# Performance work log

Measured on AMD Instinct MI355X. Metric: run time of the kernel, lower is better.

## Reference

```python
import jax, jax.numpy as jnp
import numpy as np

EPS = 1e-5      # BatchNorm1d eps
THETA = 1.0     # spike threshold
ALPHA = 5.0     # ATan surrogate alpha

@jax.custom_vjp
def atan_spike(x):
    # forward: heaviside; backward: ATan surrogate gradient
    return (x > 0).astype(x.dtype)

def _spike_fwd(x):
    return atan_spike(x), x

def _spike_bwd(x, g):
    return (g * ALPHA / (2.0 * (1.0 + (jnp.pi / 2.0 * ALPHA * x) ** 2)),)

atan_spike.defvjp(_spike_fwd, _spike_bwd)

def _lif_layer(x, W, beta_raw, gamma, bias, readout):
    # x: [T,B,J], W: [I,J]
    x = jnp.einsum('tbj,ij->tbi', x, W)
    # BatchNorm1d over (T*B) samples, per channel (training-mode batch stats)
    mean = jnp.mean(x, axis=(0, 1))
    var = jnp.var(x, axis=(0, 1))
    x = (x - mean) * jax.lax.rsqrt(var + EPS) * gamma + bias
    beta = jax.nn.sigmoid(beta_raw)
    B, I = x.shape[1], x.shape[2]
    U0 = jnp.zeros((B, I), x.dtype)
    if readout:
        def step(Ut, xt):
            Ut = beta * Ut + (1.0 - beta) * xt
            return Ut, Ut
        _, o = jax.lax.scan(step, U0, x)
    else:
        def step(carry, xt):
            Ut, St = carry
            Ut = beta * (Ut - THETA * St) + (1.0 - beta) * xt
            St = atan_spike(Ut - THETA)
            return (Ut, St), St
        _, o = jax.lax.scan(step, (U0, U0), x)
    return o  # [T,B,I]

def setup_inputs():
    key = jax.random.key(0)
    ks = jax.random.split(key, 8)
    B, T, J, H, O = 128, 512, 700, 512, 20
    def kaiming(k, out_dim, in_dim):
        # kaiming_uniform_(a=sqrt(5)) -> bound = 1/sqrt(fan_in)
        bound = 1.0 / np.sqrt(in_dim)
        return jax.random.uniform(k, (out_dim, in_dim), jnp.float32, -bound, bound)
    return {
        'x': jax.random.normal(ks[0], (B, T, J), jnp.float32),
        'W1': kaiming(ks[1], H, J),
        'beta1': jax.random.uniform(ks[2], (H,), jnp.float32, 0.0, 1.0),
        'g1': jnp.ones((H,), jnp.float32),
        'b1': jnp.zeros((H,), jnp.float32),
        'W2': kaiming(ks[3], H, H),
        'beta2': jax.random.uniform(ks[4], (H,), jnp.float32, 0.0, 1.0),
        'g2': jnp.ones((H,), jnp.float32),
        'b2': jnp.zeros((H,), jnp.float32),
        'Wr': kaiming(ks[5], O, H),
        'betar': jax.random.uniform(ks[6], (O,), jnp.float32, 0.0, 1.0),
        'gr': jnp.ones((O,), jnp.float32),
        'br': jnp.zeros((O,), jnp.float32),
    }

def reference(x, W1, beta1, g1, b1, W2, beta2, g2, b2, Wr, betar, gr, br):
    h = jnp.transpose(x, (1, 0, 2))  # [B,T,J] -> [T,B,J]
    h = _lif_layer(h, W1, beta1, g1, b1, readout=False)
    h = _lif_layer(h, W2, beta2, g2, b2, readout=False)
    h = _lif_layer(h, Wr, betar, gr, br, readout=True)
    p = jax.nn.softmax(h, axis=2)  # [T,B,O]
    return p.sum(axis=0)           # [B,O]
```

## Files before the change

### kernel.cpp

```cpp
#include <hip/hip_runtime.h>
#include <math.h>

typedef _Float16 f16_t;
typedef _Float16 f16x8 __attribute__((ext_vector_type(8)));
typedef float f32x4 __attribute__((ext_vector_type(4)));

constexpr int Bn = 128;
constexpr int Tn = 512;
constexpr int Jn = 700;
constexpr int Jp = 704;
constexpr int Hn = 512;
constexpr int On = 20;
constexpr int Mn = Bn * Tn;

#define LDS_U32(p) ((__attribute__((address_space(3))) uint32_t*)(p))
#define GLB_U32(p) ((const __attribute__((address_space(1))) uint32_t*)(p))

template <int NT, int MODE>
__global__ __launch_bounds__(512, 4) void gemm_snn(
    const f16_t* __restrict__ A, const f16_t* __restrict__ W,
    float* __restrict__ C, float* __restrict__ s_out, float* __restrict__ q_out,
    int LDA, int LDW, int KP, int pairs, int Nout, float outScale)
{
    constexpr int JT = 2 * NT;
    constexpr int ASL = (MODE == 0) ? 2 : 1;
    __shared__ __align__(16) f16_t sA[ASL * 4096];
    __shared__ __align__(16) f16_t sW[2 * NT * 4096];

    const int tid  = threadIdx.x;
    const int bm   = blockIdx.y * 128;
    const int bn   = blockIdx.x * (NT * 128);
    const int lane = tid & 63;
    const int wv   = tid >> 6;
    const int wm   = (wv & 1) * 64;
    const int wn   = (wv >> 1) * (NT * 32);
    const int fr   = lane & 15;
    const int quad = lane >> 4;
    const int srow = lane >> 2;
    const int scol = (((lane & 3) ^ ((lane >> 3) & 3)) * 8);
    const int ksw  = ((quad ^ ((fr >> 1) & 3)) * 8);

    f32x4 acc[4][JT];
#pragma unroll
    for (int i = 0; i < 4; ++i)
#pragma unroll
        for (int j = 0; j < JT; ++j) acc[i][j] = {0.f, 0.f, 0.f, 0.f};

    for (int p = 0; p < pairs; ++p) {
#pragma unroll
        for (int cc = 0; cc < ASL; ++cc) {
            const int c  = wv + cc * 8;
            const int s  = c >> 3;
            const int cr = (c & 7) * 16;
            const int kA = (MODE == 0) ? p * 64 + s * 32 : p * 32;
            const uint32_t off = __builtin_amdgcn_readfirstlane(s * 8192 + cr * 64);
            const f16_t* gp = A + (size_t)(bm + cr + srow) * LDA + kA + scol;
            __builtin_amdgcn_global_load_lds(GLB_U32(gp), LDS_U32((char*)sA + off), 16, 0, 0);
        }
#pragma unroll
        for (int cc = 0; cc < 2 * NT; ++cc) {
            const int c   = wv + cc * 8;
            const int h   = c / (NT * 8);
            const int rem = c % (NT * 8);
            const int nt  = rem >> 3;
            const int cr  = (rem & 7) * 16;
            const int kW  = (MODE == 0) ? p * 64 + h * 32 : h * KP + p * 32;
            const uint32_t off = __builtin_amdgcn_readfirstlane((h * NT + nt) * 8192 + cr * 64);
            const f16_t* gp = W + (size_t)(bn + nt * 128 + cr + srow) * LDW + kW + scol;
            __builtin_amdgcn_global_load_lds(GLB_U32(gp), LDS_U32((char*)sW + off), 16, 0, 0);
        }
        __syncthreads();

        f16x8 av[4];
#pragma unroll
        for (int h = 0; h < 2; ++h) {
            if (h == 0 || MODE == 0) {
                const int s = (MODE == 0) ? h : 0;
#pragma unroll
                for (int i = 0; i < 4; ++i)
                    av[i] = *(const f16x8*)&sA[s * 4096 + (wm + i * 16 + fr) * 32 + ksw];
            }
            f16x8 wf[JT];
#pragma unroll
            for (int jt = 0; jt < JT; ++jt) {
                const int n = wn + jt * 16 + fr;
                wf[jt] = *(const f16x8*)&sW[(h * NT + (n >> 7)) * 4096 + (n & 127) * 32 + ksw];
            }
#pragma unroll
            for (int i = 0; i < 4; ++i)
#pragma unroll
                for (int jt = 0; jt < JT; ++jt)
                    acc[i][jt] = __builtin_amdgcn_mfma_f32_16x16x32_f16(av[i], wf[jt], acc[i][jt], 0, 0, 0);
        }
        __syncthreads();
    }

#pragma unroll
    for (int jt = 0; jt < JT; ++jt) {
        const int gcol = bn + wn + jt * 16 + fr;
        float s = 0.f, q = 0.f;
        if (gcol < Nout) {
#pragma unroll
            for (int i = 0; i < 4; ++i) {
#pragma unroll
                for (int rg = 0; rg < 4; ++rg) {
                    const float v = acc[i][jt][rg] * outScale;
                    C[(size_t)(bm + wm + i * 16 + quad * 4 + rg) * Nout + gcol] = v;
                    s += v;
                    q += v * v;
                }
            }
        }
        s += __shfl_xor(s, 16); s += __shfl_xor(s, 32);
        q += __shfl_xor(q, 16); q += __shfl_xor(q, 32);
        if (quad == 0 && gcol < Nout) {
            atomicAdd(&s_out[gcol], s);
            atomicAdd(&q_out[gcol], q);
        }
    }
}

__global__ __launch_bounds__(256) void conv_a1(const float* __restrict__ x,
                                               f16_t* __restrict__ A1) {
    const int idx = blockIdx.x * 256 + threadIdx.x;
    const int m = idx / 88, g = idx % 88;
    const int k8 = g * 8;
    const float* rp = x + (size_t)m * Jn + k8;
    float f[8];
    if (k8 + 8 <= Jn) {
        const float4 v0 = *(const float4*)rp;
        const float4 v1 = *(const float4*)(rp + 4);
        f[0] = v0.x; f[1] = v0.y; f[2] = v0.z; f[3] = v0.w;
        f[4] = v1.x; f[5] = v1.y; f[6] = v1.z; f[7] = v1.w;
    } else {
#pragma unroll
        for (int e = 0; e < 8; ++e) f[e] = (k8 + e < Jn) ? rp[e] : 0.f;
    }
    f16x8 hv;
#pragma unroll
    for (int e = 0; e < 8; ++e) hv[e] = (f16_t)(f[e] * 32.f);
    *(f16x8*)&A1[(size_t)m * Jp + k8] = hv;
}

__global__ __launch_bounds__(256) void conv_w1(const float* __restrict__ Wsrc,
                                               f16_t* __restrict__ Wo) {
    const int idx = blockIdx.x * 256 + threadIdx.x;
    if (idx >= Hn * 88) return;
    const int n = idx / 88, g = idx % 88;
    const int k8 = g * 8;
    const float* rp = Wsrc + (size_t)n * Jn + k8;
    f16x8 hv;
#pragma unroll
    for (int e = 0; e < 8; ++e) {
        const float f = (k8 + e < Jn) ? rp[e] : 0.f;
        hv[e] = (f16_t)(f * 64.f);
    }
    *(f16x8*)&Wo[(size_t)n * Jp + k8] = hv;
}

__global__ __launch_bounds__(256) void split_w(const float* __restrict__ Wsrc,
                                               f16_t* __restrict__ Wo,
                                               int N, int K, int KP, int NP) {
    const int idx = blockIdx.x * 256 + threadIdx.x;
    if (idx >= NP * KP) return;
    const int n = idx / KP, k = idx % KP;
    const float f = (n < N && k < K) ? Wsrc[(size_t)n * K + k] * 64.f : 0.f;
    const f16_t hi = (f16_t)f;
    const f16_t lo = (f16_t)(f - (float)hi);
    Wo[(size_t)n * (2 * KP) + k] = hi;
    Wo[(size_t)n * (2 * KP) + KP + k] = lo;
}

__global__ __launch_bounds__(256) void lif_scan1(const float* __restrict__ X,
                                                 f16_t* __restrict__ S_out,
                                                 const float* __restrict__ sums,
                                                 const float* __restrict__ sumsq,
                                                 const float* __restrict__ beta_raw,
                                                 const float* __restrict__ gamma,
                                                 const float* __restrict__ bias) {
    const int gid = blockIdx.x * 256 + threadIdx.x;
    const int b = gid >> 9;
    const int i = gid & 511;

    const float invM = 1.f / (float)Mn;
    const float mean = sums[i] * invM;
    const float var  = sumsq[i] * invM - mean * mean;
    const float inv  = rsqrtf(var + 1e-5f);
    const float g    = gamma[i] * inv;
    const float bi   = bias[i] - mean * g;
    const float bt   = 1.f / (1.f + expf(-beta_raw[i]));
    const float ob   = 1.f - bt;

    const float* xp = X + (size_t)b * Tn * Hn + i;
    f16_t* sp = S_out + (size_t)b * Tn * Hn + i;

    float U = 0.f, Sp = 0.f;
#pragma unroll 8
    for (int t = 0; t < Tn; ++t) {
        const float xt = xp[(size_t)t * Hn] * g + bi;
        U = bt * (U - Sp) + ob * xt;
        Sp = (U > 1.0f) ? 1.0f : 0.0f;
        sp[(size_t)t * Hn] = (f16_t)Sp;
    }
}

__global__ __launch_bounds__(256) void readout_kernel(const float* __restrict__ A,
                                                      const float* __restrict__ sums,
                                                      const float* __restrict__ sumsq,
                                                      const float* __restrict__ beta_raw,
                                                      const float* __restrict__ gamma,
                                                      const float* __restrict__ bias,
                                                      float* __restrict__ out) {
    __shared__ float xs[Tn * On];
    __shared__ float gsh[On], bsh[On], betash[On];
    __shared__ float red[4][On];

    const int b = blockIdx.x;
    const int tid = threadIdx.x;

    if (tid < On) {
        const float invM = 1.f / (float)Mn;
        const float mean = sums[tid] * invM;
        const float var = sumsq[tid] * invM - mean * mean;
        const float inv = rsqrtf(var + 1e-5f);
        const float g = gamma[tid] * inv;
        gsh[tid] = g;
        bsh[tid] = bias[tid] - mean * g;
        betash[tid] = 1.f / (1.f + expf(-beta_raw[tid]));
    }
    __syncthreads();

    const float* Ab = A + (size_t)b * Tn * On;
    for (int idx = tid; idx < Tn * On; idx += 256) {
        const int o = idx % On;
        xs[idx] = Ab[idx] * gsh[o] + bsh[o];
    }
    __syncthreads();

    if (tid < On) {
        const float beta = betash[tid], omb = 1.f - beta;
        float U = 0.f;
        for (int t = 0; t < Tn; ++t) {
            U = beta * U + omb * xs[t * On + tid];
            xs[t * On + tid] = U;
        }
    }
    __syncthreads();

    float part[On];
#pragma unroll
    for (int o = 0; o < On; ++o) part[o] = 0.f;

    for (int t = tid; t < Tn; t += 256) {
        float v[On];
        float m = -1e30f;
#pragma unroll
        for (int o = 0; o < On; ++o) {
            v[o] = xs[t * On + o];
            m = fmaxf(m, v[o]);
        }
        float s = 0.f;
#pragma unroll
        for (int o = 0; o < On; ++o) {
            v[o] = expf(v[o] - m);
            s += v[o];
        }
        const float rs = 1.f / s;
#pragma unroll
        for (int o = 0; o < On; ++o) part[o] += v[o] * rs;
    }

#pragma unroll
    for (int o = 0; o < On; ++o) {
#pragma unroll
        for (int off = 32; off > 0; off >>= 1) part[o] += __shfl_down(part[o], off);
    }
    const int lane = tid & 63, wid = tid >> 6;
    if (lane == 0) {
#pragma unroll
        for (int o = 0; o < On; ++o) red[wid][o] = part[o];
    }
    __syncthreads();
    if (tid < On) out[b * On + tid] = red[0][tid] + red[1][tid] + red[2][tid] + red[3][tid];
}

extern "C" void kernel_launch(void* const* d_in, const int* in_sizes, int n_in,
                              void* d_out, int out_size, void* d_ws, size_t ws_size,
                              hipStream_t stream) {
    const float* x   = (const float*)d_in[0];
    const float* W1  = (const float*)d_in[1];
    const float* be1 = (const float*)d_in[2];
    const float* g1  = (const float*)d_in[3];
    const float* b1  = (const float*)d_in[4];
    const float* W2  = (const float*)d_in[5];
    const float* be2 = (const float*)d_in[6];
    const float* b2g = (const float*)d_in[7];
    const float* b2  = (const float*)d_in[8];
    const float* Wr  = (const float*)d_in[9];
    const float* ber = (const float*)d_in[10];
    const float* gr  = (const float*)d_in[11];
    const float* br  = (const float*)d_in[12];
    float* out = (float*)d_out;

    char* ws = (char*)d_ws;
    const size_t r0Bytes   = (size_t)Mn * Jp * sizeof(f16_t);
    const size_t bufCBytes = (size_t)Mn * Hn * sizeof(float);
    f16_t* A1   = (f16_t*)ws;
    f16_t* bufS = (f16_t*)ws;
    float* bufC = (float*)(ws + r0Bytes);
    char*  p    = ws + r0Bytes + bufCBytes;
    float* bufR = (float*)p;              p += (size_t)Mn * On * sizeof(float);
    f16_t* W1h  = (f16_t*)p;              p += (size_t)Hn * Jp * sizeof(f16_t);
    f16_t* W2s  = (f16_t*)p;              p += (size_t)Hn * (2 * Hn) * sizeof(f16_t);
    f16_t* Wrs  = (f16_t*)p;              p += (size_t)128 * (2 * Hn) * sizeof(f16_t);
    float* stats = (float*)p;
    float* s1 = stats;       float* q1 = s1 + Hn;
    float* s2 = q1 + Hn;     float* q2 = s2 + Hn;
    float* s3 = q2 + Hn;     float* q3 = s3 + 32;

    hipMemsetAsync(stats, 0, (4 * Hn + 64) * sizeof(float), stream);

    conv_a1<<<(Mn * 88) / 256, 256, 0, stream>>>(x, A1);
    conv_w1<<<(Hn * 88 + 255) / 256, 256, 0, stream>>>(W1, W1h);
    split_w<<<(Hn * Hn + 255) / 256, 256, 0, stream>>>(W2, W2s, Hn, Hn, Hn, Hn);
    split_w<<<(128 * Hn + 255) / 256, 256, 0, stream>>>(Wr, Wrs, On, Hn, Hn, 128);

    gemm_snn<2, 0><<<dim3(2, Mn / 128), 512, 0, stream>>>(A1, W1h, bufC, s1, q1,
        Jp, Jp, 0, Jp / 64, Hn, 1.f / 2048.f);
    lif_scan1<<<Mn * Hn / (512 * 256), 256, 0, stream>>>(bufC, bufS, s1, q1, be1, g1, b1);

    gemm_snn<2, 1><<<dim3(2, Mn / 128), 512, 0, stream>>>(bufS, W2s, bufC, s2, q2,
        Hn, 2 * Hn, Hn, Hn / 32, Hn, 1.f / 64.f);
    lif_scan1<<<Mn * Hn / (512 * 256), 256, 0, stream>>>(bufC, bufS, s2, q2, be2, b2g, b2);

    gemm_snn<1, 1><<<dim3(1, Mn / 128), 512, 0, stream>>>(bufS, Wrs, bufR, s3, q3,
        Hn, 2 * Hn, Hn, Hn / 32, On, 1.f / 64.f);
    readout_kernel<<<Bn, 256, 0, stream>>>(bufR, s3, q3, ber, gr, br, out);
}
```

Measured before the change: 588.7 us.

## Drop hi/lo weight split, unscaled f16 GEMMs, swizzled grid, paired-channel LIF scan

```diff
diff --git a/kernel.cpp b/kernel.cpp
--- a/kernel.cpp
+++ b/kernel.cpp
@@ -2,6 +2,7 @@
 #include <math.h>
 
 typedef _Float16 f16_t;
+typedef _Float16 f16x2 __attribute__((ext_vector_type(2)));
 typedef _Float16 f16x8 __attribute__((ext_vector_type(8)));
 typedef float f32x4 __attribute__((ext_vector_type(4)));
 
@@ -16,20 +17,28 @@
 #define LDS_U32(p) ((__attribute__((address_space(3))) uint32_t*)(p))
 #define GLB_U32(p) ((const __attribute__((address_space(1))) uint32_t*)(p))
 
-template <int NT, int MODE>
-__global__ __launch_bounds__(512, 4) void gemm_snn(
+template <int NT, bool SWZ>
+__global__ __launch_bounds__(512, 4) void gemm_f16(
     const f16_t* __restrict__ A, const f16_t* __restrict__ W,
     float* __restrict__ C, float* __restrict__ s_out, float* __restrict__ q_out,
-    int LDA, int LDW, int KP, int pairs, int Nout, float outScale)
+    int LDA, int LDW, int pairs, int Nout)
 {
     constexpr int JT = 2 * NT;
-    constexpr int ASL = (MODE == 0) ? 2 : 1;
-    __shared__ __align__(16) f16_t sA[ASL * 4096];
+    __shared__ __align__(16) f16_t sA[2 * 4096];
     __shared__ __align__(16) f16_t sW[2 * NT * 4096];
 
+    int bx, by;
+    if (SWZ) {
+        const int g = blockIdx.x;
+        by = (g >> 4) * 8 + (g & 7);
+        bx = (g >> 3) & 1;
+    } else {
+        bx = blockIdx.x;
+        by = blockIdx.y;
+    }
     const int tid  = threadIdx.x;
-    const int bm   = blockIdx.y * 128;
-    const int bn   = blockIdx.x * (NT * 128);
+    const int bm   = by * 128;
+    const int bn   = bx * (NT * 128);
     const int lane = tid & 63;
     const int wv   = tid >> 6;
     const int wm   = (wv & 1) * 64;
@@ -48,11 +57,11 @@
 
     for (int p = 0; p < pairs; ++p) {
 #pragma unroll
-        for (int cc = 0; cc < ASL; ++cc) {
+        for (int cc = 0; cc < 2; ++cc) {
             const int c  = wv + cc * 8;
             const int s  = c >> 3;
             const int cr = (c & 7) * 16;
-            const int kA = (MODE == 0) ? p * 64 + s * 32 : p * 32;
+            const int kA = p * 64 + s * 32;
             const uint32_t off = __builtin_amdgcn_readfirstlane(s * 8192 + cr * 64);
             const f16_t* gp = A + (size_t)(bm + cr + srow) * LDA + kA + scol;
             __builtin_amdgcn_global_load_lds(GLB_U32(gp), LDS_U32((char*)sA + off), 16, 0, 0);
@@ -64,22 +73,19 @@
             const int rem = c % (NT * 8);
             const int nt  = rem >> 3;
             const int cr  = (rem & 7) * 16;
-            const int kW  = (MODE == 0) ? p * 64 + h * 32 : h * KP + p * 32;
+            const int kW  = p * 64 + h * 32;
             const uint32_t off = __builtin_amdgcn_readfirstlane((h * NT + nt) * 8192 + cr * 64);
             const f16_t* gp = W + (size_t)(bn + nt * 128 + cr + srow) * LDW + kW + scol;
             __builtin_amdgcn_global_load_lds(GLB_U32(gp), LDS_U32((char*)sW + off), 16, 0, 0);
         }
         __syncthreads();
 
-        f16x8 av[4];
 #pragma unroll
         for (int h = 0; h < 2; ++h) {
-            if (h == 0 || MODE == 0) {
-                const int s = (MODE == 0) ? h : 0;
-#pragma unroll
-                for (int i = 0; i < 4; ++i)
-                    av[i] = *(const f16x8*)&sA[s * 4096 + (wm + i * 16 + fr) * 32 + ksw];
-            }
+            f16x8 av[4];
+#pragma unroll
+            for (int i = 0; i < 4; ++i)
+                av[i] = *(const f16x8*)&sA[h * 4096 + (wm + i * 16 + fr) * 32 + ksw];
             f16x8 wf[JT];
 #pragma unroll
             for (int jt = 0; jt < JT; ++jt) {
@@ -104,7 +110,7 @@
             for (int i = 0; i < 4; ++i) {
 #pragma unroll
                 for (int rg = 0; rg < 4; ++rg) {
-                    const float v = acc[i][jt][rg] * outScale;
+                    const float v = acc[i][jt][rg];
                     C[(size_t)(bm + wm + i * 16 + quad * 4 + rg) * Nout + gcol] = v;
                     s += v;
                     q += v * v;
@@ -120,8 +126,8 @@
     }
 }
 
-__global__ __launch_bounds__(256) void conv_a1(const float* __restrict__ x,
-                                               f16_t* __restrict__ A1) {
+__global__ __launch_bounds__(256) void conv_x(const float* __restrict__ x,
+                                              f16_t* __restrict__ A1) {
     const int idx = blockIdx.x * 256 + threadIdx.x;
     const int m = idx / 88, g = idx % 88;
     const int k8 = g * 8;
@@ -138,69 +144,69 @@
     }
     f16x8 hv;
 #pragma unroll
-    for (int e = 0; e < 8; ++e) hv[e] = (f16_t)(f[e] * 32.f);
+    for (int e = 0; e < 8; ++e) hv[e] = (f16_t)f[e];
     *(f16x8*)&A1[(size_t)m * Jp + k8] = hv;
 }
 
-__global__ __launch_bounds__(256) void conv_w1(const float* __restrict__ Wsrc,
-                                               f16_t* __restrict__ Wo) {
+__global__ __launch_bounds__(256) void conv_w(const float* __restrict__ Wsrc,
+                                              f16_t* __restrict__ Wo,
+                                              int N, int K, int KP, int NP) {
     const int idx = blockIdx.x * 256 + threadIdx.x;
-    if (idx >= Hn * 88) return;
-    const int n = idx / 88, g = idx % 88;
+    if (idx >= NP * (KP / 8)) return;
+    const int n = idx / (KP / 8), g = idx % (KP / 8);
     const int k8 = g * 8;
-    const float* rp = Wsrc + (size_t)n * Jn + k8;
     f16x8 hv;
 #pragma unroll
     for (int e = 0; e < 8; ++e) {
-        const float f = (k8 + e < Jn) ? rp[e] : 0.f;
-        hv[e] = (f16_t)(f * 64.f);
-    }
-    *(f16x8*)&Wo[(size_t)n * Jp + k8] = hv;
-}
-
-__global__ __launch_bounds__(256) void split_w(const float* __restrict__ Wsrc,
-                                               f16_t* __restrict__ Wo,
-                                               int N, int K, int KP, int NP) {
-    const int idx = blockIdx.x * 256 + threadIdx.x;
-    if (idx >= NP * KP) return;
-    const int n = idx / KP, k = idx % KP;
-    const float f = (n < N && k < K) ? Wsrc[(size_t)n * K + k] * 64.f : 0.f;
-    const f16_t hi = (f16_t)f;
-    const f16_t lo = (f16_t)(f - (float)hi);
-    Wo[(size_t)n * (2 * KP) + k] = hi;
-    Wo[(size_t)n * (2 * KP) + KP + k] = lo;
-}
-
-__global__ __launch_bounds__(256) void lif_scan1(const float* __restrict__ X,
-                                                 f16_t* __restrict__ S_out,
-                                                 const float* __restrict__ sums,
-                                                 const float* __restrict__ sumsq,
-                                                 const float* __restrict__ beta_raw,
-                                                 const float* __restrict__ gamma,
-                                                 const float* __restrict__ bias) {
+        const float f = (n < N && k8 + e < K) ? Wsrc[(size_t)n * K + k8 + e] : 0.f;
+        hv[e] = (f16_t)f;
+    }
+    *(f16x8*)&Wo[(size_t)n * KP + k8] = hv;
+}
+
+__global__ __launch_bounds__(256) void lif_scan(const float* __restrict__ X,
+                                                f16_t* __restrict__ S_out,
+                                                const float* __restrict__ sums,
+                                                const float* __restrict__ sumsq,
+                                                const float* __restrict__ beta_raw,
+                                                const float* __restrict__ gamma,
+                                                const float* __restrict__ bias) {
     const int gid = blockIdx.x * 256 + threadIdx.x;
-    const int b = gid >> 9;
-    const int i = gid & 511;
-
-    const float invM = 1.f / (float)Mn;
-    const float mean = sums[i] * invM;
-    const float var  = sumsq[i] * invM - mean * mean;
-    const float inv  = rsqrtf(var + 1e-5f);
-    const float g    = gamma[i] * inv;
-    const float bi   = bias[i] - mean * g;
-    const float bt   = 1.f / (1.f + expf(-beta_raw[i]));
-    const float ob   = 1.f - bt;
-
-    const float* xp = X + (size_t)b * Tn * Hn + i;
-    f16_t* sp = S_out + (size_t)b * Tn * Hn + i;
-
-    float U = 0.f, Sp = 0.f;
+    const int b  = gid >> 8;
+    const int cq = gid & 255;
+    const int i0 = cq * 2;
+
+    float g[2], bi[2], bt[2], ob[2];
+#pragma unroll
+    for (int e = 0; e < 2; ++e) {
+        const int i = i0 + e;
+        const float invM = 1.f / (float)Mn;
+        const float mean = sums[i] * invM;
+        const float var  = sumsq[i] * invM - mean * mean;
+        const float inv  = rsqrtf(var + 1e-5f);
+        g[e]  = gamma[i] * inv;
+        bi[e] = bias[i] - mean * g[e];
+        bt[e] = 1.f / (1.f + expf(-beta_raw[i]));
+        ob[e] = 1.f - bt[e];
+    }
+
+    const float2* Xp = (const float2*)(X + (size_t)b * Tn * Hn) + cq;
+    f16x2* Sp2 = (f16x2*)(S_out + (size_t)b * Tn * Hn) + cq;
+
+    float U[2] = {0.f, 0.f}, Sp[2] = {0.f, 0.f};
 #pragma unroll 8
     for (int t = 0; t < Tn; ++t) {
-        const float xt = xp[(size_t)t * Hn] * g + bi;
-        U = bt * (U - Sp) + ob * xt;
-        Sp = (U > 1.0f) ? 1.0f : 0.0f;
-        sp[(size_t)t * Hn] = (f16_t)Sp;
+        const float2 v = Xp[(size_t)t * (Hn / 2)];
+        const float vf[2] = {v.x, v.y};
+        f16x2 so;
+#pragma unroll
+        for (int e = 0; e < 2; ++e) {
+            const float xt = vf[e] * g[e] + bi[e];
+            U[e] = bt[e] * (U[e] - Sp[e]) + ob[e] * xt;
+            Sp[e] = (U[e] > 1.0f) ? 1.0f : 0.0f;
+            so[e] = (f16_t)Sp[e];
+        }
+        Sp2[(size_t)t * (Hn / 2)] = so;
     }
 }
 
@@ -311,8 +317,8 @@
     char*  p    = ws + r0Bytes + bufCBytes;
     float* bufR = (float*)p;              p += (size_t)Mn * On * sizeof(float);
     f16_t* W1h  = (f16_t*)p;              p += (size_t)Hn * Jp * sizeof(f16_t);
-    f16_t* W2s  = (f16_t*)p;              p += (size_t)Hn * (2 * Hn) * sizeof(f16_t);
-    f16_t* Wrs  = (f16_t*)p;              p += (size_t)128 * (2 * Hn) * sizeof(f16_t);
+    f16_t* W2h  = (f16_t*)p;              p += (size_t)Hn * Hn * sizeof(f16_t);
+    f16_t* Wrh  = (f16_t*)p;              p += (size_t)128 * Hn * sizeof(f16_t);
     float* stats = (float*)p;
     float* s1 = stats;       float* q1 = s1 + Hn;
     float* s2 = q1 + Hn;     float* q2 = s2 + Hn;
@@ -320,20 +326,20 @@
 
     hipMemsetAsync(stats, 0, (4 * Hn + 64) * sizeof(float), stream);
 
-    conv_a1<<<(Mn * 88) / 256, 256, 0, stream>>>(x, A1);
-    conv_w1<<<(Hn * 88 + 255) / 256, 256, 0, stream>>>(W1, W1h);
-    split_w<<<(Hn * Hn + 255) / 256, 256, 0, stream>>>(W2, W2s, Hn, Hn, Hn, Hn);
-    split_w<<<(128 * Hn + 255) / 256, 256, 0, stream>>>(Wr, Wrs, On, Hn, Hn, 128);
-
-    gemm_snn<2, 0><<<dim3(2, Mn / 128), 512, 0, stream>>>(A1, W1h, bufC, s1, q1,
-        Jp, Jp, 0, Jp / 64, Hn, 1.f / 2048.f);
-    lif_scan1<<<Mn * Hn / (512 * 256), 256, 0, stream>>>(bufC, bufS, s1, q1, be1, g1, b1);
-
-    gemm_snn<2, 1><<<dim3(2, Mn / 128), 512, 0, stream>>>(bufS, W2s, bufC, s2, q2,
-        Hn, 2 * Hn, Hn, Hn / 32, Hn, 1.f / 64.f);
-    lif_scan1<<<Mn * Hn / (512 * 256), 256, 0, stream>>>(bufC, bufS, s2, q2, be2, b2g, b2);
-
-    gemm_snn<1, 1><<<dim3(1, Mn / 128), 512, 0, stream>>>(bufS, Wrs, bufR, s3, q3,
-        Hn, 2 * Hn, Hn, Hn / 32, On, 1.f / 64.f);
+    conv_x<<<(Mn * 88) / 256, 256, 0, stream>>>(x, A1);
+    conv_w<<<(Hn * 88 + 255) / 256, 256, 0, stream>>>(W1, W1h, Hn, Jn, Jp, Hn);
+    conv_w<<<(Hn * 64 + 255) / 256, 256, 0, stream>>>(W2, W2h, Hn, Hn, Hn, Hn);
+    conv_w<<<(128 * 64 + 255) / 256, 256, 0, stream>>>(Wr, Wrh, On, Hn, Hn, 128);
+
+    gemm_f16<2, true><<<2 * (Mn / 128), 512, 0, stream>>>(A1, W1h, bufC, s1, q1,
+        Jp, Jp, Jp / 64, Hn);
+    lif_scan<<<(Bn * Hn / 2) / 256, 256, 0, stream>>>(bufC, bufS, s1, q1, be1, g1, b1);
+
+    gemm_f16<2, true><<<2 * (Mn / 128), 512, 0, stream>>>(bufS, W2h, bufC, s2, q2,
+        Hn, Hn, Hn / 64, Hn);
+    lif_scan<<<(Bn * Hn / 2) / 256, 256, 0, stream>>>(bufC, bufS, s2, q2, be2, b2g, b2);
+
+    gemm_f16<1, false><<<dim3(1, Mn / 128), 512, 0, stream>>>(bufS, Wrh, bufR, s3, q3,
+        Hn, Hn, Hn / 64, On);
     readout_kernel<<<Bn, 256, 0, stream>>>(bufR, s3, q3, ber, gr, br, out);
 }
```

Measured after the change: 562.3 us. 4.5% less time.
